# Optimization experiments

Measured on AMD Instinct MI355X. Metric: run time of the kernel, lower is better.

## Reference

```python
import jax, jax.numpy as jnp
import numpy as np

N = 100000
E = 1600000
D = 64
BETA = 1.0


def setup_inputs() -> dict:
    key = jax.random.key(0)
    ks = jax.random.split(key, 6)
    x = jax.random.normal(ks[0], (N, D), dtype=jnp.float32)
    edge_index = jax.random.randint(ks[1], (2, E), 0, N, dtype=jnp.int64)
    s = 1.0 / np.sqrt(D)
    Wm = jax.random.uniform(ks[2], (D, D), jnp.float32, -s, s)
    bm = jax.random.uniform(ks[3], (D,), jnp.float32, -s, s)
    Wr = jax.random.uniform(ks[4], (D, D), jnp.float32, -s, s)
    br = jax.random.uniform(ks[5], (D,), jnp.float32, -s, s)
    return {"x": x, "edge_index": edge_index, "Wm": Wm, "bm": bm, "Wr": Wr, "br": br}


def reference(x, edge_index, Wm, bm, Wr, br):
    row, col = edge_index[0], edge_index[1]
    # gather source features and apply message linear: [E, D]
    messages = x[row] @ Wm + bm
    scores = BETA * messages.mean(axis=-1)  # [E]
    # edge softmax over incoming edges of each destination node (col)
    seg_max = jax.ops.segment_max(scores, col, num_segments=N)  # [N]
    ex = jnp.exp(scores - seg_max[col])  # [E]
    seg_sum = jax.ops.segment_sum(ex, col, num_segments=N)  # [N]
    weights = ex / seg_sum[col]  # [E]
    # weighted scatter-add back to destinations
    out = jax.ops.segment_sum(messages * weights[:, None], col, num_segments=N)
    return out + (x @ Wr + br)
```

## Files before the change

kernel.cpp:

```cpp
#include <hip/hip_runtime.h>
#include <math.h>

#define N_NODES 100000
#define DIM 64
#define N_EDGES 1600000

#define NBF 782
#define BK_NODES 128
#define CAP 3072

#define SC_CHUNK 8192
#define SC_BLOCKS ((N_EDGES + SC_CHUNK - 1) / SC_CHUNK)

#define GEMM_BLOCKS ((N_NODES / 16 + 15) / 16)
#define PH_BLOCKS (SC_BLOCKS + GEMM_BLOCKS)

typedef _Float16 half8 __attribute__((ext_vector_type(8)));
typedef _Float16 half4 __attribute__((ext_vector_type(4)));
typedef float f32x4 __attribute__((ext_vector_type(4)));

__global__ __launch_bounds__(1024) void k_phase(
        const float* __restrict__ x,
        const float* __restrict__ Wm, const float* __restrict__ bm,
        const float* __restrict__ Wr, const float* __restrict__ br,
        const int* __restrict__ row, const int* __restrict__ col,
        int* __restrict__ cursor, unsigned int* __restrict__ pairs,
        _Float16* __restrict__ Mh, float* __restrict__ es,
        float* __restrict__ out) {
    __shared__ int cnt[NBF];
    __shared__ int base_l[NBF];
    __shared__ int base_g[NBF];
    __shared__ int wsum[16];
    __shared__ unsigned int stage[SC_CHUNK];
    __shared__ unsigned short stage_bk[SC_CHUNK];

    const int t = threadIdx.x;
    const int lane = t & 63;
    const int wid = t >> 6;

    if (blockIdx.x < SC_BLOCKS) {
        const int start = blockIdx.x * SC_CHUNK;
        const int mEnd = min(N_EDGES, start + SC_CHUNK);

        for (int i = t; i < NBF; i += 1024) cnt[i] = 0;
        __syncthreads();

        int rr[8], cc[8], lr[8];
#pragma unroll
        for (int k = 0; k < 8; ++k) {
            const int idx = start + k * 1024 + t;
            if (idx < mEnd) {
                cc[k] = col[idx];
                rr[k] = row[idx];
                lr[k] = atomicAdd(&cnt[cc[k] >> 7], 1);
            }
        }
        __syncthreads();

        const int v = (t < NBF) ? cnt[t] : 0;
        int inc = v;
#pragma unroll
        for (int o = 1; o < 64; o <<= 1) {
            const int u = __shfl_up(inc, o, 64);
            if (lane >= o) inc += u;
        }
        if (lane == 63) wsum[wid] = inc;
        __syncthreads();
        if (wid == 0) {
            const int wv = (lane < 16) ? wsum[lane] : 0;
            int winc = wv;
#pragma unroll
            for (int o = 1; o < 16; o <<= 1) {
                const int u = __shfl_up(winc, o, 64);
                if (lane >= o) winc += u;
            }
            if (lane < 16) wsum[lane] = winc - wv;
        }
        __syncthreads();
        if (t < NBF) {
            base_l[t] = inc - v + wsum[wid];
            if (v > 0) base_g[t] = atomicAdd(&cursor[t], v);
        }
        __syncthreads();

#pragma unroll
        for (int k = 0; k < 8; ++k) {
            const int idx = start + k * 1024 + t;
            if (idx < mEnd) {
                const int bk = cc[k] >> 7;
                const int slot = base_l[bk] + lr[k];
                stage[slot] = ((unsigned int)rr[k] << 7) | (unsigned int)(cc[k] & 127);
                stage_bk[slot] = (unsigned short)bk;
            }
        }
        __syncthreads();

        const int m = mEnd - start;
        for (int i = t; i < m; i += 1024) {
            const int bk = stage_bk[i];
            const int gslot = base_g[bk] + (i - base_l[bk]);
            if (gslot < CAP) pairs[(size_t)bk * CAP + gslot] = stage[i];
        }
        return;
    }

    const int wave = (blockIdx.x - SC_BLOCKS) * 16 + wid;
    if (wave >= N_NODES / 16) return;
    const int quad = lane >> 4;
    const int l15 = lane & 15;
    const int row0 = wave * 16;

    half8 bfrag[8][2];
#pragma unroll
    for (int ct = 0; ct < 8; ++ct) {
        const float* W = (ct < 4) ? Wm : Wr;
        const int c = (ct & 3) * 16 + l15;
#pragma unroll
        for (int kc = 0; kc < 2; ++kc) {
            half8 f;
#pragma unroll
            for (int j = 0; j < 8; ++j)
                f[j] = (_Float16)W[(kc * 32 + quad * 8 + j) * DIM + c];
            bfrag[ct][kc] = f;
        }
    }

    half8 afrag[2];
#pragma unroll
    for (int kc = 0; kc < 2; ++kc) {
        const float* xp = x + (size_t)(row0 + l15) * DIM + kc * 32 + quad * 8;
        const float4 x0 = *(const float4*)xp;
        const float4 x1 = *(const float4*)(xp + 4);
        half8 f;
        f[0] = (_Float16)x0.x; f[1] = (_Float16)x0.y;
        f[2] = (_Float16)x0.z; f[3] = (_Float16)x0.w;
        f[4] = (_Float16)x1.x; f[5] = (_Float16)x1.y;
        f[6] = (_Float16)x1.z; f[7] = (_Float16)x1.w;
        afrag[kc] = f;
    }

    f32x4 acc[8];
#pragma unroll
    for (int ct = 0; ct < 8; ++ct) {
        f32x4 a = {0.f, 0.f, 0.f, 0.f};
        a = __builtin_amdgcn_mfma_f32_16x16x32_f16(afrag[0], bfrag[ct][0], a, 0, 0, 0);
        a = __builtin_amdgcn_mfma_f32_16x16x32_f16(afrag[1], bfrag[ct][1], a, 0, 0, 0);
        acc[ct] = a;
    }

    float rsum[4] = {0.f, 0.f, 0.f, 0.f};
#pragma unroll
    for (int ct = 0; ct < 8; ++ct) {
        const float bias = (ct < 4) ? bm[(ct & 3) * 16 + l15]
                                    : br[(ct & 3) * 16 + l15];
#pragma unroll
        for (int r = 0; r < 4; ++r) {
            const float v = acc[ct][r] + bias;
            const size_t idx = (size_t)(row0 + quad * 4 + r) * DIM + (ct & 3) * 16 + l15;
            if (ct < 4) {
                Mh[idx] = (_Float16)v;
                rsum[r] += v;
            } else {
                out[idx] = v;
            }
        }
    }
#pragma unroll
    for (int o = 1; o <= 8; o <<= 1) {
#pragma unroll
        for (int r = 0; r < 4; ++r) rsum[r] += __shfl_xor(rsum[r], o, 64);
    }
    if (l15 == 0) {
#pragma unroll
        for (int r = 0; r < 4; ++r)
            es[row0 + quad * 4 + r] = __expf(rsum[r] * (1.0f / DIM));
    }
}

__global__ __launch_bounds__(512) void k_bucket_gather(
        const unsigned int* __restrict__ pairs, const int* __restrict__ cursor,
        const float* __restrict__ es, const half4* __restrict__ Mh4,
        float4* __restrict__ out4) {
    __shared__ unsigned int sorted[CAP];
    __shared__ int cnt[BK_NODES];
    __shared__ int off[BK_NODES];
    const int b = blockIdx.x;
    const int t = threadIdx.x;
    const int m = min(cursor[b], CAP);
    const size_t base = (size_t)b * CAP;

    if (t < BK_NODES) cnt[t] = 0;
    __syncthreads();

    unsigned int pk[6];
    int rk[6];
#pragma unroll
    for (int k = 0; k < 6; ++k) {
        const int i = k * 512 + t;
        if (i < m) {
            pk[k] = pairs[base + i];
            rk[k] = atomicAdd(&cnt[pk[k] & 127u], 1);
        }
    }
    __syncthreads();

    int v = 0;
    if (t < BK_NODES) {
        v = cnt[t];
        off[t] = v;
    }
    __syncthreads();
    for (int o = 1; o < BK_NODES; o <<= 1) {
        int add = 0;
        if (t < BK_NODES && t >= o) add = off[t - o];
        __syncthreads();
        if (t < BK_NODES) off[t] += add;
        __syncthreads();
    }
    if (t < BK_NODES) off[t] -= v;
    __syncthreads();

#pragma unroll
    for (int k = 0; k < 6; ++k) {
        const int i = k * 512 + t;
        if (i < m) sorted[off[pk[k] & 127u] + rk[k]] = pk[k];
    }
    __syncthreads();

    const int g = t >> 4;
    const int gl = t & 15;
    for (int c = g; c < BK_NODES; c += 32) {
        const int node = b * BK_NODES + c;
        if (node >= N_NODES) break;
        const int s0i = off[c];
        const int len = cnt[c];
        if (len == 0) continue;

        float a0x = 0.f, a0y = 0.f, a0z = 0.f, a0w = 0.f, l0 = 0.f;
        float a1x = 0.f, a1y = 0.f, a1z = 0.f, a1w = 0.f, l1 = 0.f;
        int j = 0;
        for (; j + 1 < len; j += 2) {
            const int s0 = (int)(sorted[s0i + j] >> 7);
            const int s1 = (int)(sorted[s0i + j + 1] >> 7);
            const float w0 = es[s0];
            const float w1 = es[s1];
            const half4 m0 = Mh4[(size_t)s0 * 16 + gl];
            const half4 m1 = Mh4[(size_t)s1 * 16 + gl];
            l0 += w0; l1 += w1;
            a0x = fmaf(w0, (float)m0[0], a0x); a0y = fmaf(w0, (float)m0[1], a0y);
            a0z = fmaf(w0, (float)m0[2], a0z); a0w = fmaf(w0, (float)m0[3], a0w);
            a1x = fmaf(w1, (float)m1[0], a1x); a1y = fmaf(w1, (float)m1[1], a1y);
            a1z = fmaf(w1, (float)m1[2], a1z); a1w = fmaf(w1, (float)m1[3], a1w);
        }
        if (j < len) {
            const int s0 = (int)(sorted[s0i + j] >> 7);
            const float w0 = es[s0];
            const half4 m0 = Mh4[(size_t)s0 * 16 + gl];
            l0 += w0;
            a0x = fmaf(w0, (float)m0[0], a0x); a0y = fmaf(w0, (float)m0[1], a0y);
            a0z = fmaf(w0, (float)m0[2], a0z); a0w = fmaf(w0, (float)m0[3], a0w);
        }
        const float inv = 1.0f / (l0 + l1);
        float4 r = out4[(size_t)node * 16 + gl];
        r.x = fmaf(a0x + a1x, inv, r.x);
        r.y = fmaf(a0y + a1y, inv, r.y);
        r.z = fmaf(a0z + a1z, inv, r.z);
        r.w = fmaf(a0w + a1w, inv, r.w);
        out4[(size_t)node * 16 + gl] = r;
    }
}

extern "C" void kernel_launch(void* const* d_in, const int* in_sizes, int n_in,
                              void* d_out, int out_size, void* d_ws, size_t ws_size,
                              hipStream_t stream) {
    const float* x  = (const float*)d_in[0];
    const int*   ei = (const int*)d_in[1];
    const float* Wm = (const float*)d_in[2];
    const float* bm = (const float*)d_in[3];
    const float* Wr = (const float*)d_in[4];
    const float* br = (const float*)d_in[5];
    float* out = (float*)d_out;
    const int* row = ei;
    const int* col = ei + N_EDGES;

    char* ws = (char*)d_ws;
    _Float16* Mh    = (_Float16*)ws;     ws += (size_t)N_NODES * DIM * sizeof(_Float16);
    float* es       = (float*)ws;        ws += (size_t)N_NODES * sizeof(float);
    int* cursor     = (int*)ws;          ws += (size_t)1024 * sizeof(int);
    unsigned int* pairs = (unsigned int*)ws; ws += (size_t)NBF * CAP * sizeof(unsigned int);

    hipMemsetAsync(cursor, 0, NBF * sizeof(int), stream);

    k_phase<<<PH_BLOCKS, 1024, 0, stream>>>(x, Wm, bm, Wr, br, row, col,
                                            cursor, pairs, Mh, es, out);
    k_bucket_gather<<<NBF, 512, 0, stream>>>(pairs, cursor, es,
                                             (const half4*)Mh, (float4*)out);
}
```

Baseline: 160.1 us.

## Halve destination bucket size, use multi-segment scan, and unroll gather by four

Destination buckets shrink from 128 to 64 nodes, which doubles the bucket count. This lets the gather kernel launch twice as many blocks with smaller shared sort buffers, and its local prefix scan becomes a single-wave shuffle scan. The binning phase now scans bucket counts in 1024-wide segments and reuses the cnt array to hold the global offsets, which frees the base_g shared array. The gather inner loop is unrolled to four edges so more loads are in flight. In exchange the scatter phase does more atomics on the global cursor and more scan passes, and each bucket is capped at 1408 entries, so heavy buckets risk overflow.

```diff
diff --git a/kernel.cpp b/kernel.cpp
--- a/kernel.cpp
+++ b/kernel.cpp
@@ -5,9 +5,9 @@
 #define DIM 64
 #define N_EDGES 1600000
 
-#define NBF 782
-#define BK_NODES 128
-#define CAP 3072
+#define NBF 1563
+#define BK_NODES 64
+#define CAP 1408
 
 #define SC_CHUNK 8192
 #define SC_BLOCKS ((N_EDGES + SC_CHUNK - 1) / SC_CHUNK)
@@ -29,8 +29,8 @@
         float* __restrict__ out) {
     __shared__ int cnt[NBF];
     __shared__ int base_l[NBF];
-    __shared__ int base_g[NBF];
     __shared__ int wsum[16];
+    __shared__ int segtot;
     __shared__ unsigned int stage[SC_CHUNK];
     __shared__ unsigned short stage_bk[SC_CHUNK];
 
@@ -52,44 +52,51 @@
             if (idx < mEnd) {
                 cc[k] = col[idx];
                 rr[k] = row[idx];
-                lr[k] = atomicAdd(&cnt[cc[k] >> 7], 1);
+                lr[k] = atomicAdd(&cnt[cc[k] >> 6], 1);
             }
         }
         __syncthreads();
 
-        const int v = (t < NBF) ? cnt[t] : 0;
-        int inc = v;
-#pragma unroll
-        for (int o = 1; o < 64; o <<= 1) {
-            const int u = __shfl_up(inc, o, 64);
-            if (lane >= o) inc += u;
-        }
-        if (lane == 63) wsum[wid] = inc;
-        __syncthreads();
-        if (wid == 0) {
-            const int wv = (lane < 16) ? wsum[lane] : 0;
-            int winc = wv;
-#pragma unroll
-            for (int o = 1; o < 16; o <<= 1) {
-                const int u = __shfl_up(winc, o, 64);
-                if (lane >= o) winc += u;
-            }
-            if (lane < 16) wsum[lane] = winc - wv;
-        }
-        __syncthreads();
-        if (t < NBF) {
-            base_l[t] = inc - v + wsum[wid];
-            if (v > 0) base_g[t] = atomicAdd(&cursor[t], v);
-        }
-        __syncthreads();
+        int segbase = 0;
+        for (int s = 0; s < NBF; s += 1024) {
+            const int i = s + t;
+            const int v = (i < NBF) ? cnt[i] : 0;
+            int inc = v;
+#pragma unroll
+            for (int o = 1; o < 64; o <<= 1) {
+                const int u = __shfl_up(inc, o, 64);
+                if (lane >= o) inc += u;
+            }
+            if (lane == 63) wsum[wid] = inc;
+            __syncthreads();
+            if (wid == 0) {
+                const int wv = (lane < 16) ? wsum[lane] : 0;
+                int winc = wv;
+#pragma unroll
+                for (int o = 1; o < 16; o <<= 1) {
+                    const int u = __shfl_up(winc, o, 64);
+                    if (lane >= o) winc += u;
+                }
+                if (lane < 16) wsum[lane] = winc - wv;
+            }
+            __syncthreads();
+            const int excl = segbase + inc - v + wsum[wid];
+            if (i < NBF) {
+                base_l[i] = excl;
+                if (v > 0) cnt[i] = atomicAdd(&cursor[i], v) - excl;
+            }
+            if (t == 1023) segtot = excl + v;
+            __syncthreads();
+            segbase = segtot;
+        }
 
 #pragma unroll
         for (int k = 0; k < 8; ++k) {
             const int idx = start + k * 1024 + t;
             if (idx < mEnd) {
-                const int bk = cc[k] >> 7;
+                const int bk = cc[k] >> 6;
                 const int slot = base_l[bk] + lr[k];
-                stage[slot] = ((unsigned int)rr[k] << 7) | (unsigned int)(cc[k] & 127);
+                stage[slot] = ((unsigned int)rr[k] << 6) | (unsigned int)(cc[k] & 63);
                 stage_bk[slot] = (unsigned short)bk;
             }
         }
@@ -98,7 +105,7 @@
         const int m = mEnd - start;
         for (int i = t; i < m; i += 1024) {
             const int bk = stage_bk[i];
-            const int gslot = base_g[bk] + (i - base_l[bk]);
+            const int gslot = cnt[bk] + i;
             if (gslot < CAP) pairs[(size_t)bk * CAP + gslot] = stage[i];
         }
         return;
@@ -186,44 +193,42 @@
     __shared__ int off[BK_NODES];
     const int b = blockIdx.x;
     const int t = threadIdx.x;
+    const int lane = t & 63;
+    const int wid = t >> 6;
     const int m = min(cursor[b], CAP);
     const size_t base = (size_t)b * CAP;
 
     if (t < BK_NODES) cnt[t] = 0;
     __syncthreads();
 
-    unsigned int pk[6];
-    int rk[6];
-#pragma unroll
-    for (int k = 0; k < 6; ++k) {
+    unsigned int pk[3];
+    int rk[3];
+#pragma unroll
+    for (int k = 0; k < 3; ++k) {
         const int i = k * 512 + t;
         if (i < m) {
             pk[k] = pairs[base + i];
-            rk[k] = atomicAdd(&cnt[pk[k] & 127u], 1);
+            rk[k] = atomicAdd(&cnt[pk[k] & 63u], 1);
         }
     }
     __syncthreads();
 
-    int v = 0;
-    if (t < BK_NODES) {
-        v = cnt[t];
-        off[t] = v;
+    if (wid == 0) {
+        const int v = cnt[lane];
+        int inc = v;
+#pragma unroll
+        for (int o = 1; o < 64; o <<= 1) {
+            const int u = __shfl_up(inc, o, 64);
+            if (lane >= o) inc += u;
+        }
+        off[lane] = inc - v;
     }
     __syncthreads();
-    for (int o = 1; o < BK_NODES; o <<= 1) {
-        int add = 0;
-        if (t < BK_NODES && t >= o) add = off[t - o];
-        __syncthreads();
-        if (t < BK_NODES) off[t] += add;
-        __syncthreads();
-    }
-    if (t < BK_NODES) off[t] -= v;
-    __syncthreads();
-
-#pragma unroll
-    for (int k = 0; k < 6; ++k) {
+
+#pragma unroll
+    for (int k = 0; k < 3; ++k) {
         const int i = k * 512 + t;
-        if (i < m) sorted[off[pk[k] & 127u] + rk[k]] = pk[k];
+        if (i < m) sorted[off[pk[k] & 63u] + rk[k]] = pk[k];
     }
     __syncthreads();
 
@@ -238,34 +243,46 @@
 
         float a0x = 0.f, a0y = 0.f, a0z = 0.f, a0w = 0.f, l0 = 0.f;
         float a1x = 0.f, a1y = 0.f, a1z = 0.f, a1w = 0.f, l1 = 0.f;
+        float a2x = 0.f, a2y = 0.f, a2z = 0.f, a2w = 0.f, l2 = 0.f;
+        float a3x = 0.f, a3y = 0.f, a3z = 0.f, a3w = 0.f, l3 = 0.f;
         int j = 0;
-        for (; j + 1 < len; j += 2) {
-            const int s0 = (int)(sorted[s0i + j] >> 7);
-            const int s1 = (int)(sorted[s0i + j + 1] >> 7);
+        for (; j + 3 < len; j += 4) {
+            const int s0 = (int)(sorted[s0i + j] >> 6);
+            const int s1 = (int)(sorted[s0i + j + 1] >> 6);
+            const int s2 = (int)(sorted[s0i + j + 2] >> 6);
+            const int s3 = (int)(sorted[s0i + j + 3] >> 6);
             const float w0 = es[s0];
             const float w1 = es[s1];
+            const float w2 = es[s2];
+            const float w3 = es[s3];
             const half4 m0 = Mh4[(size_t)s0 * 16 + gl];
             const half4 m1 = Mh4[(size_t)s1 * 16 + gl];
-            l0 += w0; l1 += w1;
+            const half4 m2 = Mh4[(size_t)s2 * 16 + gl];
+            const half4 m3 = Mh4[(size_t)s3 * 16 + gl];
+            l0 += w0; l1 += w1; l2 += w2; l3 += w3;
             a0x = fmaf(w0, (float)m0[0], a0x); a0y = fmaf(w0, (float)m0[1], a0y);
             a0z = fmaf(w0, (float)m0[2], a0z); a0w = fmaf(w0, (float)m0[3], a0w);
             a1x = fmaf(w1, (float)m1[0], a1x); a1y = fmaf(w1, (float)m1[1], a1y);
             a1z = fmaf(w1, (float)m1[2], a1z); a1w = fmaf(w1, (float)m1[3], a1w);
-        }
-        if (j < len) {
-            const int s0 = (int)(sorted[s0i + j] >> 7);
+            a2x = fmaf(w2, (float)m2[0], a2x); a2y = fmaf(w2, (float)m2[1], a2y);
+            a2z = fmaf(w2, (float)m2[2], a2z); a2w = fmaf(w2, (float)m2[3], a2w);
+            a3x = fmaf(w3, (float)m3[0], a3x); a3y = fmaf(w3, (float)m3[1], a3y);
+            a3z = fmaf(w3, (float)m3[2], a3z); a3w = fmaf(w3, (float)m3[3], a3w);
+        }
+        for (; j < len; ++j) {
+            const int s0 = (int)(sorted[s0i + j] >> 6);
             const float w0 = es[s0];
             const half4 m0 = Mh4[(size_t)s0 * 16 + gl];
             l0 += w0;
             a0x = fmaf(w0, (float)m0[0], a0x); a0y = fmaf(w0, (float)m0[1], a0y);
             a0z = fmaf(w0, (float)m0[2], a0z); a0w = fmaf(w0, (float)m0[3], a0w);
         }
-        const float inv = 1.0f / (l0 + l1);
+        const float inv = 1.0f / (l0 + l1 + l2 + l3);
         float4 r = out4[(size_t)node * 16 + gl];
-        r.x = fmaf(a0x + a1x, inv, r.x);
-        r.y = fmaf(a0y + a1y, inv, r.y);
-        r.z = fmaf(a0z + a1z, inv, r.z);
-        r.w = fmaf(a0w + a1w, inv, r.w);
+        r.x = fmaf(a0x + a1x + a2x + a3x, inv, r.x);
+        r.y = fmaf(a0y + a1y + a2y + a3y, inv, r.y);
+        r.z = fmaf(a0z + a1z + a2z + a3z, inv, r.z);
+        r.w = fmaf(a0w + a1w + a2w + a3w, inv, r.w);
         out4[(size_t)node * 16 + gl] = r;
     }
 }
@@ -286,7 +303,7 @@
     char* ws = (char*)d_ws;
     _Float16* Mh    = (_Float16*)ws;     ws += (size_t)N_NODES * DIM * sizeof(_Float16);
     float* es       = (float*)ws;        ws += (size_t)N_NODES * sizeof(float);
-    int* cursor     = (int*)ws;          ws += (size_t)1024 * sizeof(int);
+    int* cursor     = (int*)ws;          ws += (size_t)2048 * sizeof(int);
     unsigned int* pairs = (unsigned int*)ws; ws += (size_t)NBF * CAP * sizeof(unsigned int);
 
     hipMemsetAsync(cursor, 0, NBF * sizeof(int), stream);
```

New measurement: 153.4 us. 1.04x faster.
